# Kernel optimization log

Hardware: AMD Instinct MI355X
Metric: run time of the kernel (lower is better)

Reference implementation:

```python
import jax, jax.numpy as jnp
import numpy as np

SEQ_LENS = np.array([512, 1024, 1536, 2048, 640, 896, 1280, 1792], dtype=np.int64)
T = int(SEQ_LENS.sum())          # 9728 total tokens (cu_seq_len)
D = 2048                          # hidden_size
K = 4                             # kernel_size
GH = 256                          # generator hidden = D // 8


def setup_inputs() -> dict:
    key = jax.random.key(0)
    ks = jax.random.split(key, 6)
    return {
        "x": jax.random.normal(ks[0], (T, D), dtype=jnp.float32),
        "conv_state": jax.random.normal(ks[1], (len(SEQ_LENS), D, K - 1), dtype=jnp.float32),
        "generator_input": jax.random.normal(ks[2], (T, D), dtype=jnp.float32),
        "seq_lens": jnp.asarray(SEQ_LENS),
        "w1": jax.random.normal(ks[3], (D, GH), dtype=jnp.float32) * (1.0 / np.sqrt(D)),
        "w2": jax.random.normal(ks[4], (GH, D * K), dtype=jnp.float32) * (1.0 / np.sqrt(GH)),
        "b2": jax.random.normal(ks[5], (D * K,), dtype=jnp.float32) * 0.01,
    }


def reference(x, conv_state, generator_input, seq_lens, w1, w2, b2):
    lens = np.asarray(seq_lens)              # static ragged lengths
    B = lens.shape[0]
    L = int(lens.max())
    k = conv_state.shape[2] + 1              # kernel_size
    d = x.shape[1]
    t = x.shape[0]

    # ---- kernel generator: Linear -> SiLU -> Linear(+bias), per token ----
    h = jax.nn.silu(generator_input @ w1)                    # (T, GH)
    kern = (h @ w2 + b2).reshape(t, d, k)                    # (T, D, K)

    # ---- left-pad each ragged sequence; prepend conv_state (k-1 steps) ----
    offs = np.concatenate([[0], np.cumsum(lens)])
    x_rows, k_rows = [], []
    for i in range(B):                                        # B is small & static
        xi = jnp.concatenate([conv_state[i].T, x[offs[i]:offs[i + 1]]], axis=0)  # (len_i+k-1, D)
        x_rows.append(jnp.pad(xi, ((L + k - 1 - xi.shape[0], 0), (0, 0))))
        ki = kern[offs[i]:offs[i + 1]]                        # (len_i, D, K)
        k_rows.append(jnp.pad(ki, ((L - int(lens[i]), 0), (0, 0), (0, 0))))
    x_pad = jnp.stack(x_rows)                                 # (B, L+k-1, D)
    k_pad = jnp.stack(k_rows)                                 # (B, L, D, K)

    # new conv state = last k-1 timesteps of the (state+tokens) sequence
    new_conv_state = jnp.swapaxes(x_pad[:, -(k - 1):, :], 1, 2)  # (B, D, k-1)

    # ---- causal dynamic depthwise conv: window j uses x_pad[j:j+k] ----
    out_pad = x_pad[:, 0:L, :] * k_pad[..., 0]
    for kk in range(1, k):                                    # k=4, static tiny loop
        out_pad = out_pad + x_pad[:, kk:kk + L, :] * k_pad[..., kk]  # (B, L, D)

    # ---- un-pad back to ragged layout, apply SiLU ----
    out = jnp.concatenate([out_pad[i, L - int(lens[i]):] for i in range(B)], axis=0)  # (T, D)
    return jax.nn.silu(out), new_conv_state
```

## Files before the change

kernel.cpp:

```cpp
#include <hip/hip_runtime.h>
#include <cstdint>
#include <cstddef>

typedef __attribute__((ext_vector_type(8))) short bf16x8;
typedef __attribute__((ext_vector_type(4))) unsigned short u16x4;
typedef __attribute__((ext_vector_type(4))) unsigned u32x4;
typedef __attribute__((ext_vector_type(4))) float f32x4;
typedef unsigned short u16;

#define T_TOT 9728
#define DDIM  2048
#define GHN   256
#define NSEQ  8

__device__ __constant__ int OFFS[NSEQ + 1] = {0, 512, 1536, 3072, 5120, 5760, 6656, 7936, 9728};

__device__ __forceinline__ u16 f2bf(float f) {
  union { float f; unsigned u; } v; v.f = f;
  unsigned r = v.u + 0x7FFFu + ((v.u >> 16) & 1u);
  return (u16)(r >> 16);
}
__device__ __forceinline__ float silu_f(float v) {
  return v / (1.0f + __expf(-v));
}

__device__ __forceinline__ void pin_reg(bf16x8& v) {
  u32x4& u = reinterpret_cast<u32x4&>(v);
  asm volatile("" : "+v"(u));
}

__device__ __forceinline__ void gload_lds16(const u16* src, u16* dst) {
  __builtin_amdgcn_global_load_lds(
      (__attribute__((address_space(1))) void*)src,
      (__attribute__((address_space(3))) void*)dst,
      16, 0, 0);
}

__global__ __launch_bounds__(256)
void transpose_bf16_k(const float* __restrict__ in, u16* __restrict__ out, int R, int C) {
  __shared__ float tile[64][65];
  const int c0 = blockIdx.x * 64, r0 = blockIdx.y * 64;
  const int tid = threadIdx.x;
  const int lc = tid & 63, lr = tid >> 6;
#pragma unroll
  for (int p = 0; p < 16; ++p) {
    int r = lr + p * 4;
    tile[r][lc] = in[(size_t)(r0 + r) * C + c0 + lc];
  }
  __syncthreads();
#pragma unroll
  for (int p = 0; p < 16; ++p) {
    int c = lr + p * 4;
    out[(size_t)(c0 + c) * R + r0 + lc] = f2bf(tile[lc][c]);
  }
}

__global__ __launch_bounds__(256, 4)
void gemm1_silu(const float* __restrict__ gi, const u16* __restrict__ w1T,
                u16* __restrict__ h) {
  __shared__ u16 A[32][72];
  const int tid = threadIdx.x;
  const int lane = tid & 63, wid = tid >> 6;
  const int l15 = lane & 15, l4 = lane >> 4;
  const int t0 = blockIdx.x * 32;
  const int nb = wid * 64;

  f32x4 acc[2][4] = {};

  for (int k0 = 0; k0 < DDIM; k0 += 64) {
#pragma unroll
    for (int j = 0; j < 2; ++j) {
      int idx = tid + j * 256;
      int m = idx >> 4, f4 = idx & 15;
      f32x4 v = *reinterpret_cast<const f32x4*>(&gi[(size_t)(t0 + m) * DDIM + k0 + f4 * 4]);
      u16x4 b;
      b[0] = f2bf(v[0]); b[1] = f2bf(v[1]); b[2] = f2bf(v[2]); b[3] = f2bf(v[3]);
      *reinterpret_cast<u16x4*>(&A[m][f4 * 4]) = b;
    }
    __syncthreads();
#pragma unroll
    for (int ks = 0; ks < 2; ++ks) {
      bf16x8 af[2], bfr[4];
#pragma unroll
      for (int mi = 0; mi < 2; ++mi)
        af[mi] = *reinterpret_cast<const bf16x8*>(&A[mi * 16 + l15][ks * 32 + 8 * l4]);
#pragma unroll
      for (int ni = 0; ni < 4; ++ni)
        bfr[ni] = *reinterpret_cast<const bf16x8*>(
            &w1T[(size_t)(nb + ni * 16 + l15) * DDIM + k0 + ks * 32 + 8 * l4]);
#pragma unroll
      for (int mi = 0; mi < 2; ++mi)
#pragma unroll
        for (int ni = 0; ni < 4; ++ni)
          acc[mi][ni] = __builtin_amdgcn_mfma_f32_16x16x32_bf16(af[mi], bfr[ni], acc[mi][ni], 0, 0, 0);
    }
    __syncthreads();
  }

#pragma unroll
  for (int mi = 0; mi < 2; ++mi)
#pragma unroll
    for (int ni = 0; ni < 4; ++ni)
#pragma unroll
      for (int r = 0; r < 4; ++r) {
        float v = silu_f(acc[mi][ni][r]);
        int token = t0 + mi * 16 + l4 * 4 + r;
        int c = nb + ni * 16 + l15;
        int pos = ((((c >> 3) ^ (token & 7)) << 3) | (c & 7));
        h[(size_t)token * GHN + pos] = f2bf(v);
      }
}

__global__ __launch_bounds__(256, 3)
void gemm2_conv(const u16* __restrict__ h, const u16* __restrict__ w2T,
                const float* __restrict__ b2, const float* __restrict__ x,
                const float* __restrict__ cs, float* __restrict__ out) {
  __shared__ u16 H[64 * 256];
  __shared__ float Ot[64 * 33];
  const int tid = threadIdx.x;
  const int lane = tid & 63, wid = tid >> 6;
  const int l15 = lane & 15, l4 = lane >> 4;
  const int colwave = blockIdx.y * 128 + wid * 32;
  const int d0 = blockIdx.y * 32;
  const int tg = blockIdx.x;

  const int ocol = colwave + 4 * (l15 >> 1) + 2 * (l15 & 1);

  bf16x8 bw[8][2];
#pragma unroll
  for (int ks = 0; ks < 8; ++ks)
#pragma unroll
    for (int ni = 0; ni < 2; ++ni)
      bw[ks][ni] = *reinterpret_cast<const bf16x8*>(
          w2T + (size_t)(ocol + ni) * GHN + ks * 32 + l4 * 8);
#pragma unroll
  for (int ks = 0; ks < 8; ++ks)
#pragma unroll
    for (int ni = 0; ni < 2; ++ni)
      pin_reg(bw[ks][ni]);

  float b2v[2];
#pragma unroll
  for (int ni = 0; ni < 2; ++ni) b2v[ni] = b2[ocol + ni];

  const int d = (colwave >> 2) + (l15 >> 1);
  const int dloc = wid * 8 + (l15 >> 1);
  const int k0 = 2 * (l15 & 1);
  const int par = lane & 1;

  {
    const u16* hb = h + (size_t)(tg * 4) * 64 * GHN;
#pragma unroll
    for (int p = 0; p < 8; ++p)
      gload_lds16(hb + (size_t)(p * 256 + tid) * 8, &H[(p * 256 + tid) * 8]);
  }
  __syncthreads();

  for (int it = 0; it < 4; ++it) {
    const int t0 = (tg * 4 + it) * 64;

    f32x4 acc[4][2] = {};
#pragma unroll
    for (int ks = 0; ks < 8; ++ks) {
#pragma unroll
      for (int mi = 0; mi < 4; ++mi) {
        int m = mi * 16 + l15;
        int g = ks * 4 + l4;
        bf16x8 af = *reinterpret_cast<const bf16x8*>(&H[m * 256 + ((g ^ (m & 7)) << 3)]);
#pragma unroll
        for (int ni = 0; ni < 2; ++ni)
          acc[mi][ni] = __builtin_amdgcn_mfma_f32_16x16x32_bf16(af, bw[ks][ni], acc[mi][ni], 0, 0, 0);
      }
    }

    __syncthreads();

    if (it < 3) {
      const u16* hb = h + (size_t)(t0 + 64) * GHN;
#pragma unroll
      for (int p = 0; p < 8; ++p)
        gload_lds16(hb + (size_t)(p * 256 + tid) * 8, &H[(p * 256 + tid) * 8]);
    }

    int iseq = 0;
    while (OFFS[iseq + 1] <= t0) ++iseq;
    const int seq_start = OFFS[iseq];

#pragma unroll
    for (int mi = 0; mi < 4; ++mi) {
      const int base = t0 + mi * 16 + l4 * 4;
      float xw[5];
#pragma unroll
      for (int j = 0; j < 5; ++j) {
        int src = base + j + k0 - 3;
        xw[j] = (src >= seq_start)
                    ? x[(size_t)src * DDIM + d]
                    : cs[((size_t)iseq * DDIM + d) * 3 + (src - seq_start + 3)];
      }
#pragma unroll
      for (int r = 0; r < 4; ++r) {
        float partial = (acc[mi][0][r] + b2v[0]) * xw[r] +
                        (acc[mi][1][r] + b2v[1]) * xw[r + 1];
        float tot = partial + __shfl_xor(partial, 1);
        if ((r >> 1) == par)
          Ot[(mi * 16 + l4 * 4 + r) * 33 + dloc] = silu_f(tot);
      }
    }

    __syncthreads();

    {
      const int trow = tid >> 2, tq = tid & 3;
      f32x4 o0 = *reinterpret_cast<const f32x4*>(&Ot[trow * 33 + tq * 8]);
      f32x4 o1 = *reinterpret_cast<const f32x4*>(&Ot[trow * 33 + tq * 8 + 4]);
      float* op = out + (size_t)(t0 + trow) * DDIM + d0 + tq * 8;
      *reinterpret_cast<f32x4*>(op) = o0;
      *reinterpret_cast<f32x4*>(op + 4) = o1;
    }

    __syncthreads();
  }
}

__global__ __launch_bounds__(256)
void tail_state(const float* __restrict__ x, float* __restrict__ out2) {
  int idx = blockIdx.x * 256 + threadIdx.x;
  int i = idx / (DDIM * 3);
  int rem = idx - i * (DDIM * 3);
  int d = rem / 3, m = rem - d * 3;
  int token = OFFS[i + 1] - 3 + m;
  out2[idx] = x[(size_t)token * DDIM + d];
}

extern "C" void kernel_launch(void* const* d_in, const int* in_sizes, int n_in,
                              void* d_out, int out_size, void* d_ws, size_t ws_size,
                              hipStream_t stream) {
  (void)in_sizes; (void)n_in; (void)out_size; (void)ws_size;
  const float* x  = (const float*)d_in[0];
  const float* cs = (const float*)d_in[1];
  const float* gi = (const float*)d_in[2];
  const float* w1 = (const float*)d_in[4];
  const float* w2 = (const float*)d_in[5];
  const float* b2 = (const float*)d_in[6];
  float* out = (float*)d_out;

  char* ws = (char*)d_ws;
  u16* w2T = (u16*)ws;
  u16* w1T = (u16*)(ws + 4194304);
  u16* h   = (u16*)(ws + 4194304 + 1048576);

  transpose_bf16_k<<<dim3(8192 / 64, 256 / 64), 256, 0, stream>>>(w2, w2T, GHN, DDIM * 4);
  transpose_bf16_k<<<dim3(256 / 64, 2048 / 64), 256, 0, stream>>>(w1, w1T, DDIM, GHN);
  gemm1_silu<<<T_TOT / 32, 256, 0, stream>>>(gi, w1T, h);
  gemm2_conv<<<dim3(T_TOT / 256, (DDIM * 4) / 128), 256, 0, stream>>>(h, w2T, b2, x, cs, out);
  tail_state<<<(NSEQ * DDIM * 3) / 256, 256, 0, stream>>>(x, out + (size_t)T_TOT * DDIM);
}
```

Before: 193.3 us.

## Prefetch gemm1 A tiles into registers and hoist conv input loads in gemm2

gemm1 now loads the next 64-wide slice of generator_input into registers while the MFMAs run on the current LDS tile, overlapping global latency with compute. gemm2 issues its x and conv_state loads before the MFMA loop, initialises the accumulators with the bias, and drops a redundant trailing barrier. The launch-bounds occupancy hint for gemm2 is lowered from 3 to 2 to make room for the extra live registers, which may reduce latency hiding across waves.

```diff
diff --git a/kernel.cpp b/kernel.cpp
--- a/kernel.cpp
+++ b/kernel.cpp
@@ -67,17 +67,25 @@
 
   f32x4 acc[2][4] = {};
 
+  const int m0 = tid >> 4, f40 = tid & 15;
+  const float* g0 = gi + (size_t)(t0 + m0) * DDIM + f40 * 4;
+  const float* g1 = gi + (size_t)(t0 + m0 + 16) * DDIM + f40 * 4;
+
+  f32x4 pv0 = *reinterpret_cast<const f32x4*>(g0);
+  f32x4 pv1 = *reinterpret_cast<const f32x4*>(g1);
+
   for (int k0 = 0; k0 < DDIM; k0 += 64) {
-#pragma unroll
-    for (int j = 0; j < 2; ++j) {
-      int idx = tid + j * 256;
-      int m = idx >> 4, f4 = idx & 15;
-      f32x4 v = *reinterpret_cast<const f32x4*>(&gi[(size_t)(t0 + m) * DDIM + k0 + f4 * 4]);
-      u16x4 b;
-      b[0] = f2bf(v[0]); b[1] = f2bf(v[1]); b[2] = f2bf(v[2]); b[3] = f2bf(v[3]);
-      *reinterpret_cast<u16x4*>(&A[m][f4 * 4]) = b;
-    }
-    __syncthreads();
+    u16x4 b0, b1;
+    b0[0] = f2bf(pv0[0]); b0[1] = f2bf(pv0[1]); b0[2] = f2bf(pv0[2]); b0[3] = f2bf(pv0[3]);
+    b1[0] = f2bf(pv1[0]); b1[1] = f2bf(pv1[1]); b1[2] = f2bf(pv1[2]); b1[3] = f2bf(pv1[3]);
+    __syncthreads();
+    *reinterpret_cast<u16x4*>(&A[m0][f40 * 4]) = b0;
+    *reinterpret_cast<u16x4*>(&A[m0 + 16][f40 * 4]) = b1;
+    __syncthreads();
+    if (k0 + 64 < DDIM) {
+      pv0 = *reinterpret_cast<const f32x4*>(g0 + k0 + 64);
+      pv1 = *reinterpret_cast<const f32x4*>(g1 + k0 + 64);
+    }
 #pragma unroll
     for (int ks = 0; ks < 2; ++ks) {
       bf16x8 af[2], bfr[4];
@@ -94,7 +102,6 @@
         for (int ni = 0; ni < 4; ++ni)
           acc[mi][ni] = __builtin_amdgcn_mfma_f32_16x16x32_bf16(af[mi], bfr[ni], acc[mi][ni], 0, 0, 0);
     }
-    __syncthreads();
   }
 
 #pragma unroll
@@ -111,7 +118,7 @@
       }
 }
 
-__global__ __launch_bounds__(256, 3)
+__global__ __launch_bounds__(256, 2)
 void gemm2_conv(const u16* __restrict__ h, const u16* __restrict__ w2T,
                 const float* __restrict__ b2, const float* __restrict__ x,
                 const float* __restrict__ cs, float* __restrict__ out) {
@@ -145,7 +152,7 @@
 
   const int d = (colwave >> 2) + (l15 >> 1);
   const int dloc = wid * 8 + (l15 >> 1);
-  const int k0 = 2 * (l15 & 1);
+  const int k0t = 2 * (l15 & 1);
   const int par = lane & 1;
 
   {
@@ -159,7 +166,32 @@
   for (int it = 0; it < 4; ++it) {
     const int t0 = (tg * 4 + it) * 64;
 
-    f32x4 acc[4][2] = {};
+    int iseq = 0;
+    while (OFFS[iseq + 1] <= t0) ++iseq;
+    const int seq_start = OFFS[iseq];
+
+    float xw[4][5];
+#pragma unroll
+    for (int mi = 0; mi < 4; ++mi) {
+      const int base = t0 + mi * 16 + l4 * 4;
+      const int s0 = base + k0t - 3;
+      const float* xr = x + (size_t)s0 * DDIM + d;
+      const float* cr = cs + ((size_t)iseq * DDIM + d) * 3 + (s0 - seq_start + 3);
+      xw[mi][0] = (s0 >= seq_start) ? xr[0] : cr[0];
+      xw[mi][1] = (s0 + 1 >= seq_start) ? xr[DDIM] : cr[1];
+      xw[mi][2] = (s0 + 2 >= seq_start) ? xr[2 * DDIM] : cr[2];
+      xw[mi][3] = xr[3 * DDIM];
+      xw[mi][4] = xr[4 * DDIM];
+    }
+
+    f32x4 acc[4][2];
+#pragma unroll
+    for (int mi = 0; mi < 4; ++mi)
+#pragma unroll
+      for (int ni = 0; ni < 2; ++ni) {
+        acc[mi][ni][0] = b2v[ni]; acc[mi][ni][1] = b2v[ni];
+        acc[mi][ni][2] = b2v[ni]; acc[mi][ni][3] = b2v[ni];
+      }
 #pragma unroll
     for (int ks = 0; ks < 8; ++ks) {
 #pragma unroll
@@ -182,25 +214,11 @@
         gload_lds16(hb + (size_t)(p * 256 + tid) * 8, &H[(p * 256 + tid) * 8]);
     }
 
-    int iseq = 0;
-    while (OFFS[iseq + 1] <= t0) ++iseq;
-    const int seq_start = OFFS[iseq];
-
 #pragma unroll
     for (int mi = 0; mi < 4; ++mi) {
-      const int base = t0 + mi * 16 + l4 * 4;
-      float xw[5];
-#pragma unroll
-      for (int j = 0; j < 5; ++j) {
-        int src = base + j + k0 - 3;
-        xw[j] = (src >= seq_start)
-                    ? x[(size_t)src * DDIM + d]
-                    : cs[((size_t)iseq * DDIM + d) * 3 + (src - seq_start + 3)];
-      }
 #pragma unroll
       for (int r = 0; r < 4; ++r) {
-        float partial = (acc[mi][0][r] + b2v[0]) * xw[r] +
-                        (acc[mi][1][r] + b2v[1]) * xw[r + 1];
+        float partial = acc[mi][0][r] * xw[mi][r] + acc[mi][1][r] * xw[mi][r + 1];
         float tot = partial + __shfl_xor(partial, 1);
         if ((r >> 1) == par)
           Ot[(mi * 16 + l4 * 4 + r) * 33 + dloc] = silu_f(tot);
@@ -217,8 +235,6 @@
       *reinterpret_cast<f32x4*>(op) = o0;
       *reinterpret_cast<f32x4*>(op + 4) = o1;
     }
-
-    __syncthreads();
   }
 }
 
```

Result: no change. 193.1 us (-0.1%).
